# Kernel optimization log

Measured on AMD Instinct MI355X. Metric: run time of the kernel, lower is better.

Reference implementation:

```python
import jax, jax.numpy as jnp
import numpy as np

Q = 10        # icosahedral diamonds
M = 128       # 2**dggrid_level
L = Q * M * M # 163840 icosahedral points
KS = 9        # kernel_size / knn neighbors


def setup_inputs() -> dict:
    key = jax.random.key(0)
    k1, k2, k3, k4 = jax.random.split(key, 4)
    b, c, h, w = 1, 128, 256, 512
    x = jax.random.normal(k1, (b, c, h, w), dtype=jnp.float32)
    codeskmin = jax.random.randint(k2, (L, KS), 0, h * w, dtype=jnp.int32)
    att_w = jax.random.normal(k3, (KS, 2, KS), dtype=jnp.float32) * 0.1
    att_b = jnp.zeros((KS,), dtype=jnp.float32)
    depth_w = jax.random.normal(k4, (c, KS), dtype=jnp.float32) * 0.1
    depth_b = jnp.zeros((c,), dtype=jnp.float32)
    gamma = jnp.ones((c,), dtype=jnp.float32)
    beta = jnp.zeros((c,), dtype=jnp.float32)
    return {"x": x, "codeskmin": codeskmin, "att_w": att_w, "att_b": att_b,
            "depth_w": depth_w, "depth_b": depth_b, "gamma": gamma, "beta": beta}


def reference(x, codeskmin, att_w, att_b, depth_w, depth_b, gamma, beta):
    b, c, h, w = x.shape
    xf = x.reshape(b, c, h * w)
    # KNN gather: (b, c, L, KS)
    xe = xf[:, :, codeskmin]
    # --- SpatialAttentionModule_v1 ---
    avg = jnp.mean(xe, axis=1)           # (b, L, KS)
    mx = jnp.max(xe, axis=1)             # (b, L, KS)
    feat = jnp.stack([avg, mx], axis=1)  # (b, 2, L, KS)
    # Conv2d(2 -> KS, kernel (1,KS), no pad): reduces neighbor axis fully
    att = jnp.einsum('bilk,oik->bol', feat, att_w) + att_b[None, :, None]  # (b, KS, L)
    att = jax.nn.sigmoid(att)
    att = att.transpose(0, 2, 1)[:, None, :, :]  # (b, 1, L, KS)
    xe = att * xe + xe
    # --- depthwise conv over neighbor axis ---
    out = jnp.einsum('bclk,ck->bcl', xe, depth_w) + depth_b[None, :, None]  # (b, c, L)
    # rearrange 'b c (q h w) -> (b q) c h w'
    out = out.reshape(b, c, Q, M, M).transpose(0, 2, 1, 3, 4).reshape(b * Q, c, M, M)
    # BatchNorm (training-mode batch stats)
    mean = jnp.mean(out, axis=(0, 2, 3), keepdims=True)
    var = jnp.var(out, axis=(0, 2, 3), keepdims=True)
    out = (out - mean) * jax.lax.rsqrt(var + 1e-5)
    out = out * gamma[None, :, None, None] + beta[None, :, None, None]
    # Swish
    out = out * jax.nn.sigmoid(out)
    return out
```

## Files before the change

### kernel.cpp

```cpp
#include <hip/hip_runtime.h>
#include <hip/hip_bf16.h>

#define HW 131072
#define NCH 128
#define KS 9
#define L_TOTAL 163840
#define NGRP 8
#define LPB 256

typedef float        f32x2 __attribute__((ext_vector_type(2)));
typedef float        f32x4 __attribute__((ext_vector_type(4)));
typedef unsigned int u32x2 __attribute__((ext_vector_type(2)));
typedef unsigned int u32x4 __attribute__((ext_vector_type(4)));

static __device__ __forceinline__ float bflo(unsigned int p) { return __uint_as_float(p << 16); }
static __device__ __forceinline__ float bfhi(unsigned int p) { return __uint_as_float(p & 0xffff0000u); }
static __device__ __forceinline__ unsigned short f2bf(float f) {
    unsigned int x = __float_as_uint(f);
    return (unsigned short)((x + 0x7fffu + ((x >> 16) & 1u)) >> 16);
}

__global__ __launch_bounds__(256) void transpose_x_kernel(
    const f32x4* __restrict__ xf4,
    unsigned int* __restrict__ xT,
    float2* __restrict__ meanmaxP)
{
    __shared__ unsigned short tile[128 * 128];
    __shared__ float ps[8][128];
    __shared__ float pm[8][128];
    const int tid = threadIdx.x;
    const int p0 = blockIdx.x * 128;
    const int pj = tid & 31;
    const int cg = tid >> 5;

    float s0 = 0.f, s1 = 0.f, s2 = 0.f, s3 = 0.f;
    float m0 = -3.4e38f, m1 = -3.4e38f, m2 = -3.4e38f, m3 = -3.4e38f;
    #pragma unroll 4
    for (int it = 0; it < 16; ++it) {
        const int c = cg + (it << 3);
        const f32x4 v = __builtin_nontemporal_load(&xf4[(long)c * (HW / 4) + (p0 >> 2) + pj]);
        const int pA = 4 * pj;
        tile[(pA + 0) * 128 + ((c + 2 * (pA + 0)) & 127)] = f2bf(v.x);
        tile[(pA + 1) * 128 + ((c + 2 * (pA + 1)) & 127)] = f2bf(v.y);
        tile[(pA + 2) * 128 + ((c + 2 * (pA + 2)) & 127)] = f2bf(v.z);
        tile[(pA + 3) * 128 + ((c + 2 * (pA + 3)) & 127)] = f2bf(v.w);
        s0 += v.x; s1 += v.y; s2 += v.z; s3 += v.w;
        m0 = fmaxf(m0, v.x); m1 = fmaxf(m1, v.y);
        m2 = fmaxf(m2, v.z); m3 = fmaxf(m3, v.w);
    }
    {
        const int pA = 4 * pj;
        ps[cg][pA + 0] = s0; ps[cg][pA + 1] = s1;
        ps[cg][pA + 2] = s2; ps[cg][pA + 3] = s3;
        pm[cg][pA + 0] = m0; pm[cg][pA + 1] = m1;
        pm[cg][pA + 2] = m2; pm[cg][pA + 3] = m3;
    }
    __syncthreads();

    #pragma unroll 4
    for (int it = 0; it < 16; ++it) {
        const int idx2 = it * 256 + tid;
        const int s = idx2 >> 9;
        const int rem = idx2 & 511;
        const int p = rem >> 2;
        const int dp = rem & 3;
        const int cpair = s * 8 + 2 * dp;
        const int col0 = (2 * cpair + 2 * p) & 127;
        const int col1 = (2 * cpair + 2 + 2 * p) & 127;
        u32x2 u;
        u.x = *reinterpret_cast<const unsigned int*>(&tile[p * 128 + col0]);
        u.y = *reinterpret_cast<const unsigned int*>(&tile[p * 128 + col1]);
        *(u32x2*)&xT[((long)s * HW + (p0 + p)) * 8 + 2 * dp] = u;
    }
    if (tid < 128) {
        float s = 0.f, m = -3.4e38f;
        #pragma unroll
        for (int g2 = 0; g2 < 8; ++g2) {
            s += ps[g2][tid];
            m = fmaxf(m, pm[g2][tid]);
        }
        meanmaxP[p0 + tid] = make_float2(s * 0.0078125f, m);
    }
}

__global__ __launch_bounds__(256) void mult_kernel(
    const float2* __restrict__ meanmaxP,
    const int* __restrict__ cks,
    const float* __restrict__ att_w,
    const float* __restrict__ att_b,
    unsigned int* __restrict__ rec,
    float* __restrict__ gz)
{
    __shared__ float attw[162];
    __shared__ float attb[12];
    __shared__ __align__(16) unsigned int lrec[256 * 12];
    const int tid = threadIdx.x;
    const int base_l = blockIdx.x * 256;

    if (blockIdx.x == 0) gz[tid] = 0.f;

    if (tid < 162) attw[tid] = att_w[tid];
    if (tid < KS) attb[tid] = att_b[tid];
    for (int j = tid; j < 256 * KS; j += 256) {
        const int lj = j / KS;
        lrec[lj * 12 + (j - lj * KS)] = (unsigned int)cks[(long)base_l * KS + j];
    }
    __syncthreads();

    unsigned int idx[KS];
    float mean[KS], mx[KS];
    #pragma unroll
    for (int k = 0; k < KS; ++k) {
        idx[k] = lrec[tid * 12 + k];
        const float2 mm = meanmaxP[idx[k]];
        mean[k] = mm.x; mx[k] = mm.y;
    }
    #pragma unroll
    for (int o = 0; o < KS; ++o) {
        float logit = attb[o];
        #pragma unroll
        for (int k = 0; k < KS; ++k) {
            logit = fmaf(mean[k], attw[o * 18 + k], logit);
            logit = fmaf(mx[k],   attw[o * 18 + 9 + k], logit);
        }
        const float sig = 1.0f / (1.0f + __expf(-logit));
        unsigned int u = (unsigned int)(sig * 32768.0f + 0.5f);
        if (u > 32767u) u = 32767u;
        lrec[tid * 12 + o] = idx[o] | (u << 17);
    }
    __syncthreads();

    const u32x4* lv = (const u32x4*)lrec;
    u32x4* dst = (u32x4*)(rec + (size_t)base_l * 12);
    #pragma unroll
    for (int j = 0; j < 3; ++j)
        dst[j * 256 + tid] = lv[j * 256 + tid];
}

__global__ __launch_bounds__(256, 4) void gather_kernel(
    const unsigned int* __restrict__ xT,
    const unsigned int* __restrict__ rec,
    const float* __restrict__ depth_w,
    const float* __restrict__ depth_b,
    unsigned int* __restrict__ ybuf,
    float* __restrict__ gsum, float* __restrict__ gsq)
{
    __shared__ float dwl[KS][16];
    __shared__ float dbl[16];
    __shared__ float redx[4][4][8];
    __shared__ __align__(16) unsigned short ytile[16][264];

    const int tid  = threadIdx.x;
    const int lane = tid & 63;
    const int wave = tid >> 6;
    const int g      = blockIdx.x & 7;
    const int base_l = (blockIdx.x >> 3) * LPB;
    const int qt = lane & 3;
    const int lq = lane >> 2;

    if (tid < 144) {
        int k = tid >> 4, ch = tid & 15;
        dwl[k][ch] = depth_w[(g * 16 + ch) * KS + k];
    }
    if (tid < 16) dbl[tid] = depth_b[g * 16 + tid];
    __syncthreads();

    f32x2 dw[KS][2];
    #pragma unroll
    for (int k = 0; k < KS; ++k) {
        f32x4 t = *(const f32x4*)&dwl[k][qt * 4];
        dw[k][0].x = t.x; dw[k][0].y = t.y;
        dw[k][1].x = t.z; dw[k][1].y = t.w;
    }
    f32x2 db01, db23;
    {
        f32x4 t = *(const f32x4*)&dbl[qt * 4];
        db01.x = t.x; db01.y = t.y; db23.x = t.z; db23.y = t.w;
    }

    const unsigned int* slab = xT + ((size_t)g << 20);

    f32x2 sum01 = {0.f, 0.f}, sum23 = {0.f, 0.f};
    f32x2 sq01  = {0.f, 0.f}, sq23  = {0.f, 0.f};

    #pragma unroll
    for (int b = 0; b < 4; ++b) {
        const int lloc = wave * 64 + b * 16 + lq;
        const unsigned int* rp = rec + (size_t)(base_l + lloc) * 12;
        const u32x4 r0 = __builtin_nontemporal_load((const u32x4*)rp);
        const u32x4 r1 = __builtin_nontemporal_load((const u32x4*)(rp + 4));
        const unsigned int r8 = __builtin_nontemporal_load(rp + 8);
        const unsigned int rr[KS] = {r0.x, r0.y, r0.z, r0.w,
                                     r1.x, r1.y, r1.z, r1.w, r8};

        u32x2 pv[KS];
        #pragma unroll
        for (int k = 0; k < KS; ++k)
            pv[k] = *(const u32x2*)(slab + ((rr[k] & 0x1FFFFu) << 3) + (qt << 1));

        f32x2 acc01 = db01, acc23 = db23;
        #pragma unroll
        for (int k = 0; k < KS; ++k) {
            const float mk = fmaf((float)(rr[k] >> 17), 3.0517578125e-5f, 1.0f);
            f32x2 mk2; mk2.x = mk; mk2.y = mk;
            f32x2 xa; xa.x = bflo(pv[k].x); xa.y = bfhi(pv[k].x);
            f32x2 xb; xb.x = bflo(pv[k].y); xb.y = bfhi(pv[k].y);
            acc01 = __builtin_elementwise_fma(xa * mk2, dw[k][0], acc01);
            acc23 = __builtin_elementwise_fma(xb * mk2, dw[k][1], acc23);
        }

        ytile[qt * 4 + 0][lloc] = f2bf(acc01.x);
        ytile[qt * 4 + 1][lloc] = f2bf(acc01.y);
        ytile[qt * 4 + 2][lloc] = f2bf(acc23.x);
        ytile[qt * 4 + 3][lloc] = f2bf(acc23.y);

        sum01 += acc01; sum23 += acc23;
        sq01 = __builtin_elementwise_fma(acc01, acc01, sq01);
        sq23 = __builtin_elementwise_fma(acc23, acc23, sq23);
    }

    __syncthreads();

    {
        const int ch = tid >> 4;
        const int m  = tid & 15;
        const u32x4 v0 = *(const u32x4*)&ytile[ch][m * 16];
        const u32x4 v1 = *(const u32x4*)&ytile[ch][m * 16 + 8];
        unsigned int* dst = ybuf + (size_t)(g * 16 + ch) * (L_TOTAL / 2)
                          + (base_l >> 1) + m * 8;
        *(u32x4*)dst = v0;
        *(u32x4*)(dst + 4) = v1;
    }

    #pragma unroll
    for (int s = 4; s <= 32; s <<= 1) {
        sum01.x += __shfl_xor(sum01.x, s);
        sum01.y += __shfl_xor(sum01.y, s);
        sum23.x += __shfl_xor(sum23.x, s);
        sum23.y += __shfl_xor(sum23.y, s);
        sq01.x  += __shfl_xor(sq01.x,  s);
        sq01.y  += __shfl_xor(sq01.y,  s);
        sq23.x  += __shfl_xor(sq23.x,  s);
        sq23.y  += __shfl_xor(sq23.y,  s);
    }
    if (lane < 4) {
        float* rw = &redx[wave][lane][0];
        rw[0] = sum01.x; rw[1] = sum01.y; rw[2] = sum23.x; rw[3] = sum23.y;
        rw[4] = sq01.x;  rw[5] = sq01.y;  rw[6] = sq23.x;  rw[7] = sq23.y;
    }
    __syncthreads();
    if (tid < 32) {
        const int q = tid >> 2, qq = tid & 3;
        float s = redx[0][qq][q] + redx[1][qq][q] + redx[2][qq][q] + redx[3][qq][q];
        const int ch = g * 16 + qq * 4 + (q & 3);
        float* dst = (q >= 4) ? gsq : gsum;
        atomicAdd(&dst[ch], s);
    }
}

__global__ __launch_bounds__(256) void finalize_kernel(
    const u32x4* __restrict__ ybuf,
    const float* __restrict__ gsum, const float* __restrict__ gsq,
    const float* __restrict__ gamma, const float* __restrict__ beta,
    float* __restrict__ out)
{
    const int q = blockIdx.x >> 7;
    const int c = blockIdx.x & 127;
    const int tid = threadIdx.x;

    const float invN = 1.0f / (float)L_TOTAL;
    const float m = gsum[c] * invN;
    const float var = gsq[c] * invN - m * m;
    const float sc = gamma[c] * rsqrtf(var + 1e-5f);
    const float sh = beta[c] - m * sc;

    const u32x4* src = ybuf + (size_t)c * (L_TOTAL / 8) + (size_t)q * 2048;
    float* dst = out + ((size_t)(q * NCH + c) << 14);

    #pragma unroll 2
    for (int it = 0; it < 8; ++it) {
        const int i = it * 256 + tid;
        const u32x4 v = src[i];
        f32x4 o0, o1;
        float z;
        z = fmaf(bflo(v.x), sc, sh); o0.x = z / (1.0f + __expf(-z));
        z = fmaf(bfhi(v.x), sc, sh); o0.y = z / (1.0f + __expf(-z));
        z = fmaf(bflo(v.y), sc, sh); o0.z = z / (1.0f + __expf(-z));
        z = fmaf(bfhi(v.y), sc, sh); o0.w = z / (1.0f + __expf(-z));
        z = fmaf(bflo(v.z), sc, sh); o1.x = z / (1.0f + __expf(-z));
        z = fmaf(bfhi(v.z), sc, sh); o1.y = z / (1.0f + __expf(-z));
        z = fmaf(bflo(v.w), sc, sh); o1.z = z / (1.0f + __expf(-z));
        z = fmaf(bfhi(v.w), sc, sh); o1.w = z / (1.0f + __expf(-z));
        *(f32x4*)&dst[i * 8 + 0] = o0;
        *(f32x4*)&dst[i * 8 + 4] = o1;
    }
}

extern "C" void kernel_launch(void* const* d_in, const int* in_sizes, int n_in,
                              void* d_out, int out_size, void* d_ws, size_t ws_size,
                              hipStream_t stream) {
    const f32x4* x_f4  = (const f32x4*)d_in[0];
    const int* cks     = (const int*)d_in[1];
    const float* aw    = (const float*)d_in[2];
    const float* ab    = (const float*)d_in[3];
    const float* dw    = (const float*)d_in[4];
    const float* db    = (const float*)d_in[5];
    const float* gm    = (const float*)d_in[6];
    const float* bt    = (const float*)d_in[7];

    char* ws = (char*)d_ws;
    unsigned int* xT   = (unsigned int*)ws;
    float2* meanmaxP   = (float2*)(ws + 33554432);
    unsigned int* ybuf = (unsigned int*)(ws + 34603008);
    unsigned int* rec  = (unsigned int*)(ws + 76546048);
    float* gsum        = (float*)(ws + 84410368);
    float* gsq         = gsum + NCH;

    transpose_x_kernel<<<HW / 128, 256, 0, stream>>>(x_f4, xT, meanmaxP);
    mult_kernel<<<L_TOTAL / 256, 256, 0, stream>>>(meanmaxP, cks, aw, ab, rec, gsum);
    gather_kernel<<<(L_TOTAL / LPB) * NGRP, 256, 0, stream>>>(
        xT, rec, dw, db, ybuf, gsum, gsq);
    finalize_kernel<<<1280, 256, 0, stream>>>(
        (const u32x4*)ybuf, gsum, gsq, gm, bt, (float*)d_out);
}
```

Baseline: 280.6 us.

## Merge four kernels into two cooperative persistent kernels with grid sync

```diff
diff --git a/kernel.cpp b/kernel.cpp
--- a/kernel.cpp
+++ b/kernel.cpp
@@ -1,5 +1,8 @@
 #include <hip/hip_runtime.h>
 #include <hip/hip_bf16.h>
+#include <hip/hip_cooperative_groups.h>
+
+namespace cooperative_groups_ns = cooperative_groups;
 
 #define HW 131072
 #define NCH 128
@@ -20,130 +23,150 @@
     return (unsigned short)((x + 0x7fffu + ((x >> 16) & 1u)) >> 16);
 }
 
-__global__ __launch_bounds__(256) void transpose_x_kernel(
+__global__ __launch_bounds__(256, 2) void prep_kernel(
     const f32x4* __restrict__ xf4,
     unsigned int* __restrict__ xT,
-    float2* __restrict__ meanmaxP)
-{
-    __shared__ unsigned short tile[128 * 128];
-    __shared__ float ps[8][128];
-    __shared__ float pm[8][128];
-    const int tid = threadIdx.x;
-    const int p0 = blockIdx.x * 128;
-    const int pj = tid & 31;
-    const int cg = tid >> 5;
-
-    float s0 = 0.f, s1 = 0.f, s2 = 0.f, s3 = 0.f;
-    float m0 = -3.4e38f, m1 = -3.4e38f, m2 = -3.4e38f, m3 = -3.4e38f;
-    #pragma unroll 4
-    for (int it = 0; it < 16; ++it) {
-        const int c = cg + (it << 3);
-        const f32x4 v = __builtin_nontemporal_load(&xf4[(long)c * (HW / 4) + (p0 >> 2) + pj]);
-        const int pA = 4 * pj;
-        tile[(pA + 0) * 128 + ((c + 2 * (pA + 0)) & 127)] = f2bf(v.x);
-        tile[(pA + 1) * 128 + ((c + 2 * (pA + 1)) & 127)] = f2bf(v.y);
-        tile[(pA + 2) * 128 + ((c + 2 * (pA + 2)) & 127)] = f2bf(v.z);
-        tile[(pA + 3) * 128 + ((c + 2 * (pA + 3)) & 127)] = f2bf(v.w);
-        s0 += v.x; s1 += v.y; s2 += v.z; s3 += v.w;
-        m0 = fmaxf(m0, v.x); m1 = fmaxf(m1, v.y);
-        m2 = fmaxf(m2, v.z); m3 = fmaxf(m3, v.w);
-    }
-    {
-        const int pA = 4 * pj;
-        ps[cg][pA + 0] = s0; ps[cg][pA + 1] = s1;
-        ps[cg][pA + 2] = s2; ps[cg][pA + 3] = s3;
-        pm[cg][pA + 0] = m0; pm[cg][pA + 1] = m1;
-        pm[cg][pA + 2] = m2; pm[cg][pA + 3] = m3;
-    }
-    __syncthreads();
-
-    #pragma unroll 4
-    for (int it = 0; it < 16; ++it) {
-        const int idx2 = it * 256 + tid;
-        const int s = idx2 >> 9;
-        const int rem = idx2 & 511;
-        const int p = rem >> 2;
-        const int dp = rem & 3;
-        const int cpair = s * 8 + 2 * dp;
-        const int col0 = (2 * cpair + 2 * p) & 127;
-        const int col1 = (2 * cpair + 2 + 2 * p) & 127;
-        u32x2 u;
-        u.x = *reinterpret_cast<const unsigned int*>(&tile[p * 128 + col0]);
-        u.y = *reinterpret_cast<const unsigned int*>(&tile[p * 128 + col1]);
-        *(u32x2*)&xT[((long)s * HW + (p0 + p)) * 8 + 2 * dp] = u;
-    }
-    if (tid < 128) {
-        float s = 0.f, m = -3.4e38f;
-        #pragma unroll
-        for (int g2 = 0; g2 < 8; ++g2) {
-            s += ps[g2][tid];
-            m = fmaxf(m, pm[g2][tid]);
-        }
-        meanmaxP[p0 + tid] = make_float2(s * 0.0078125f, m);
-    }
-}
-
-__global__ __launch_bounds__(256) void mult_kernel(
-    const float2* __restrict__ meanmaxP,
+    float2* __restrict__ meanmaxP,
     const int* __restrict__ cks,
     const float* __restrict__ att_w,
     const float* __restrict__ att_b,
     unsigned int* __restrict__ rec,
-    float* __restrict__ gz)
+    float* __restrict__ gz,
+    int mode)
 {
-    __shared__ float attw[162];
-    __shared__ float attb[12];
-    __shared__ __align__(16) unsigned int lrec[256 * 12];
+    __shared__ __align__(16) char smem[36864];
     const int tid = threadIdx.x;
-    const int base_l = blockIdx.x * 256;
-
-    if (blockIdx.x == 0) gz[tid] = 0.f;
-
-    if (tid < 162) attw[tid] = att_w[tid];
-    if (tid < KS) attb[tid] = att_b[tid];
-    for (int j = tid; j < 256 * KS; j += 256) {
-        const int lj = j / KS;
-        lrec[lj * 12 + (j - lj * KS)] = (unsigned int)cks[(long)base_l * KS + j];
-    }
-    __syncthreads();
-
-    unsigned int idx[KS];
-    float mean[KS], mx[KS];
-    #pragma unroll
-    for (int k = 0; k < KS; ++k) {
-        idx[k] = lrec[tid * 12 + k];
-        const float2 mm = meanmaxP[idx[k]];
-        mean[k] = mm.x; mx[k] = mm.y;
-    }
-    #pragma unroll
-    for (int o = 0; o < KS; ++o) {
-        float logit = attb[o];
-        #pragma unroll
-        for (int k = 0; k < KS; ++k) {
-            logit = fmaf(mean[k], attw[o * 18 + k], logit);
-            logit = fmaf(mx[k],   attw[o * 18 + 9 + k], logit);
-        }
-        const float sig = 1.0f / (1.0f + __expf(-logit));
-        unsigned int u = (unsigned int)(sig * 32768.0f + 0.5f);
-        if (u > 32767u) u = 32767u;
-        lrec[tid * 12 + o] = idx[o] | (u << 17);
-    }
-    __syncthreads();
-
-    const u32x4* lv = (const u32x4*)lrec;
-    u32x4* dst = (u32x4*)(rec + (size_t)base_l * 12);
-    #pragma unroll
-    for (int j = 0; j < 3; ++j)
-        dst[j * 256 + tid] = lv[j * 256 + tid];
+
+    if (mode != 1) {
+        unsigned short* tile = (unsigned short*)smem;
+        float* ps = (float*)(smem + 32768);
+        float* pm = (float*)(smem + 34816);
+        const int pj = tid & 31;
+        const int cgi = tid >> 5;
+        const int wave = tid >> 6;
+
+        if (blockIdx.x == 0) gz[tid] = 0.f;
+
+        for (int tt = 0; tt < 2; ++tt) {
+            const int p0 = (blockIdx.x * 2 + tt) * 128;
+
+            float s0 = 0.f, s1 = 0.f, s2 = 0.f, s3 = 0.f;
+            float m0 = -3.4e38f, m1 = -3.4e38f, m2 = -3.4e38f, m3 = -3.4e38f;
+            #pragma unroll 4
+            for (int it = 0; it < 16; ++it) {
+                const int c = cgi + (it << 3);
+                const f32x4 v = __builtin_nontemporal_load(
+                    &xf4[(long)c * (HW / 4) + (p0 >> 2) + pj]);
+                const int pA = 4 * pj;
+                tile[(pA + 0) * 128 + ((c + 2 * (pA + 0)) & 127)] = f2bf(v.x);
+                tile[(pA + 1) * 128 + ((c + 2 * (pA + 1)) & 127)] = f2bf(v.y);
+                tile[(pA + 2) * 128 + ((c + 2 * (pA + 2)) & 127)] = f2bf(v.z);
+                tile[(pA + 3) * 128 + ((c + 2 * (pA + 3)) & 127)] = f2bf(v.w);
+                s0 += v.x; s1 += v.y; s2 += v.z; s3 += v.w;
+                m0 = fmaxf(m0, v.x); m1 = fmaxf(m1, v.y);
+                m2 = fmaxf(m2, v.z); m3 = fmaxf(m3, v.w);
+            }
+            s0 += __shfl_xor(s0, 32); s1 += __shfl_xor(s1, 32);
+            s2 += __shfl_xor(s2, 32); s3 += __shfl_xor(s3, 32);
+            m0 = fmaxf(m0, __shfl_xor(m0, 32)); m1 = fmaxf(m1, __shfl_xor(m1, 32));
+            m2 = fmaxf(m2, __shfl_xor(m2, 32)); m3 = fmaxf(m3, __shfl_xor(m3, 32));
+            if ((tid & 32) == 0) {
+                const int pA = 4 * pj;
+                ps[wave * 128 + pA + 0] = s0; ps[wave * 128 + pA + 1] = s1;
+                ps[wave * 128 + pA + 2] = s2; ps[wave * 128 + pA + 3] = s3;
+                pm[wave * 128 + pA + 0] = m0; pm[wave * 128 + pA + 1] = m1;
+                pm[wave * 128 + pA + 2] = m2; pm[wave * 128 + pA + 3] = m3;
+            }
+            __syncthreads();
+
+            #pragma unroll 4
+            for (int it = 0; it < 16; ++it) {
+                const int idx2 = it * 256 + tid;
+                const int s = idx2 >> 9;
+                const int rem = idx2 & 511;
+                const int p = rem >> 2;
+                const int dp = rem & 3;
+                const int cpair = s * 8 + 2 * dp;
+                const int col0 = (2 * cpair + 2 * p) & 127;
+                const int col1 = (2 * cpair + 2 + 2 * p) & 127;
+                u32x2 u;
+                u.x = *reinterpret_cast<const unsigned int*>(&tile[p * 128 + col0]);
+                u.y = *reinterpret_cast<const unsigned int*>(&tile[p * 128 + col1]);
+                *(u32x2*)&xT[((long)s * HW + (p0 + p)) * 8 + 2 * dp] = u;
+            }
+            if (tid < 128) {
+                float s = ps[0 * 128 + tid] + ps[1 * 128 + tid]
+                        + ps[2 * 128 + tid] + ps[3 * 128 + tid];
+                float m = fmaxf(fmaxf(pm[0 * 128 + tid], pm[1 * 128 + tid]),
+                                fmaxf(pm[2 * 128 + tid], pm[3 * 128 + tid]));
+                meanmaxP[p0 + tid] = make_float2(s * 0.0078125f, m);
+            }
+            __syncthreads();
+        }
+    }
+
+    if (mode == 2)
+        cooperative_groups_ns::this_grid().sync();
+
+    if (mode != 0) {
+        float* attw = (float*)smem;
+        float* attb = (float*)(smem + 648);
+        unsigned int* lrec = (unsigned int*)(smem + 704);
+        const int base_l = blockIdx.x * 320;
+
+        if (tid < 162) attw[tid] = att_w[tid];
+        if (tid < KS) attb[tid] = att_b[tid];
+        for (int j = tid; j < 320 * KS; j += 256) {
+            const int lj = j / KS;
+            lrec[lj * 12 + (j - lj * KS)] = (unsigned int)cks[(long)base_l * KS + j];
+        }
+        __syncthreads();
+
+        for (int lb = 0; lb < 320; lb += 256) {
+            const int ll = lb + tid;
+            if (ll < 320) {
+                unsigned int idx[KS];
+                float mean[KS], mx[KS];
+                #pragma unroll
+                for (int k = 0; k < KS; ++k) {
+                    idx[k] = lrec[ll * 12 + k];
+                    const float2 mm = meanmaxP[idx[k]];
+                    mean[k] = mm.x; mx[k] = mm.y;
+                }
+                #pragma unroll
+                for (int o = 0; o < KS; ++o) {
+                    float logit = attb[o];
+                    #pragma unroll
+                    for (int k = 0; k < KS; ++k) {
+                        logit = fmaf(mean[k], attw[o * 18 + k], logit);
+                        logit = fmaf(mx[k],   attw[o * 18 + 9 + k], logit);
+                    }
+                    const float sig = 1.0f / (1.0f + __expf(-logit));
+                    unsigned int u = (unsigned int)(sig * 32768.0f + 0.5f);
+                    if (u > 32767u) u = 32767u;
+                    lrec[ll * 12 + o] = idx[o] | (u << 17);
+                }
+            }
+        }
+        __syncthreads();
+
+        const u32x4* lv = (const u32x4*)lrec;
+        u32x4* dst = (u32x4*)(rec + (size_t)base_l * 12);
+        for (int j = tid; j < 960; j += 256)
+            dst[j] = lv[j];
+    }
 }
 
-__global__ __launch_bounds__(256, 4) void gather_kernel(
+__global__ __launch_bounds__(256, 4) void gatherfin_kernel(
     const unsigned int* __restrict__ xT,
     const unsigned int* __restrict__ rec,
     const float* __restrict__ depth_w,
     const float* __restrict__ depth_b,
     unsigned int* __restrict__ ybuf,
-    float* __restrict__ gsum, float* __restrict__ gsq)
+    float* __restrict__ gsum, float* __restrict__ gsq,
+    const float* __restrict__ gamma, const float* __restrict__ beta,
+    float* __restrict__ out,
+    int mode)
 {
     __shared__ float dwl[KS][16];
     __shared__ float dbl[16];
@@ -153,146 +176,156 @@
     const int tid  = threadIdx.x;
     const int lane = tid & 63;
     const int wave = tid >> 6;
-    const int g      = blockIdx.x & 7;
-    const int base_l = (blockIdx.x >> 3) * LPB;
+    const int g = blockIdx.x & 7;
     const int qt = lane & 3;
     const int lq = lane >> 2;
 
-    if (tid < 144) {
-        int k = tid >> 4, ch = tid & 15;
-        dwl[k][ch] = depth_w[(g * 16 + ch) * KS + k];
-    }
-    if (tid < 16) dbl[tid] = depth_b[g * 16 + tid];
-    __syncthreads();
-
-    f32x2 dw[KS][2];
-    #pragma unroll
-    for (int k = 0; k < KS; ++k) {
-        f32x4 t = *(const f32x4*)&dwl[k][qt * 4];
-        dw[k][0].x = t.x; dw[k][0].y = t.y;
-        dw[k][1].x = t.z; dw[k][1].y = t.w;
-    }
-    f32x2 db01, db23;
-    {
-        f32x4 t = *(const f32x4*)&dbl[qt * 4];
-        db01.x = t.x; db01.y = t.y; db23.x = t.z; db23.y = t.w;
-    }
-
-    const unsigned int* slab = xT + ((size_t)g << 20);
-
-    f32x2 sum01 = {0.f, 0.f}, sum23 = {0.f, 0.f};
-    f32x2 sq01  = {0.f, 0.f}, sq23  = {0.f, 0.f};
-
-    #pragma unroll
-    for (int b = 0; b < 4; ++b) {
-        const int lloc = wave * 64 + b * 16 + lq;
-        const unsigned int* rp = rec + (size_t)(base_l + lloc) * 12;
-        const u32x4 r0 = __builtin_nontemporal_load((const u32x4*)rp);
-        const u32x4 r1 = __builtin_nontemporal_load((const u32x4*)(rp + 4));
-        const unsigned int r8 = __builtin_nontemporal_load(rp + 8);
-        const unsigned int rr[KS] = {r0.x, r0.y, r0.z, r0.w,
-                                     r1.x, r1.y, r1.z, r1.w, r8};
-
-        u32x2 pv[KS];
-        #pragma unroll
-        for (int k = 0; k < KS; ++k)
-            pv[k] = *(const u32x2*)(slab + ((rr[k] & 0x1FFFFu) << 3) + (qt << 1));
-
-        f32x2 acc01 = db01, acc23 = db23;
+    if (mode != 1) {
+        if (tid < 144) {
+            int k = tid >> 4, ch = tid & 15;
+            dwl[k][ch] = depth_w[(g * 16 + ch) * KS + k];
+        }
+        if (tid < 16) dbl[tid] = depth_b[g * 16 + tid];
+        __syncthreads();
+
+        f32x2 dw[KS][2];
         #pragma unroll
         for (int k = 0; k < KS; ++k) {
-            const float mk = fmaf((float)(rr[k] >> 17), 3.0517578125e-5f, 1.0f);
-            f32x2 mk2; mk2.x = mk; mk2.y = mk;
-            f32x2 xa; xa.x = bflo(pv[k].x); xa.y = bfhi(pv[k].x);
-            f32x2 xb; xb.x = bflo(pv[k].y); xb.y = bfhi(pv[k].y);
-            acc01 = __builtin_elementwise_fma(xa * mk2, dw[k][0], acc01);
-            acc23 = __builtin_elementwise_fma(xb * mk2, dw[k][1], acc23);
-        }
-
-        ytile[qt * 4 + 0][lloc] = f2bf(acc01.x);
-        ytile[qt * 4 + 1][lloc] = f2bf(acc01.y);
-        ytile[qt * 4 + 2][lloc] = f2bf(acc23.x);
-        ytile[qt * 4 + 3][lloc] = f2bf(acc23.y);
-
-        sum01 += acc01; sum23 += acc23;
-        sq01 = __builtin_elementwise_fma(acc01, acc01, sq01);
-        sq23 = __builtin_elementwise_fma(acc23, acc23, sq23);
-    }
-
-    __syncthreads();
-
-    {
-        const int ch = tid >> 4;
-        const int m  = tid & 15;
-        const u32x4 v0 = *(const u32x4*)&ytile[ch][m * 16];
-        const u32x4 v1 = *(const u32x4*)&ytile[ch][m * 16 + 8];
-        unsigned int* dst = ybuf + (size_t)(g * 16 + ch) * (L_TOTAL / 2)
-                          + (base_l >> 1) + m * 8;
-        *(u32x4*)dst = v0;
-        *(u32x4*)(dst + 4) = v1;
-    }
-
-    #pragma unroll
-    for (int s = 4; s <= 32; s <<= 1) {
-        sum01.x += __shfl_xor(sum01.x, s);
-        sum01.y += __shfl_xor(sum01.y, s);
-        sum23.x += __shfl_xor(sum23.x, s);
-        sum23.y += __shfl_xor(sum23.y, s);
-        sq01.x  += __shfl_xor(sq01.x,  s);
-        sq01.y  += __shfl_xor(sq01.y,  s);
-        sq23.x  += __shfl_xor(sq23.x,  s);
-        sq23.y  += __shfl_xor(sq23.y,  s);
-    }
-    if (lane < 4) {
-        float* rw = &redx[wave][lane][0];
-        rw[0] = sum01.x; rw[1] = sum01.y; rw[2] = sum23.x; rw[3] = sum23.y;
-        rw[4] = sq01.x;  rw[5] = sq01.y;  rw[6] = sq23.x;  rw[7] = sq23.y;
-    }
-    __syncthreads();
-    if (tid < 32) {
-        const int q = tid >> 2, qq = tid & 3;
-        float s = redx[0][qq][q] + redx[1][qq][q] + redx[2][qq][q] + redx[3][qq][q];
-        const int ch = g * 16 + qq * 4 + (q & 3);
-        float* dst = (q >= 4) ? gsq : gsum;
-        atomicAdd(&dst[ch], s);
-    }
-}
-
-__global__ __launch_bounds__(256) void finalize_kernel(
-    const u32x4* __restrict__ ybuf,
-    const float* __restrict__ gsum, const float* __restrict__ gsq,
-    const float* __restrict__ gamma, const float* __restrict__ beta,
-    float* __restrict__ out)
-{
-    const int q = blockIdx.x >> 7;
-    const int c = blockIdx.x & 127;
-    const int tid = threadIdx.x;
-
-    const float invN = 1.0f / (float)L_TOTAL;
-    const float m = gsum[c] * invN;
-    const float var = gsq[c] * invN - m * m;
-    const float sc = gamma[c] * rsqrtf(var + 1e-5f);
-    const float sh = beta[c] - m * sc;
-
-    const u32x4* src = ybuf + (size_t)c * (L_TOTAL / 8) + (size_t)q * 2048;
-    float* dst = out + ((size_t)(q * NCH + c) << 14);
-
-    #pragma unroll 2
-    for (int it = 0; it < 8; ++it) {
-        const int i = it * 256 + tid;
-        const u32x4 v = src[i];
-        f32x4 o0, o1;
-        float z;
-        z = fmaf(bflo(v.x), sc, sh); o0.x = z / (1.0f + __expf(-z));
-        z = fmaf(bfhi(v.x), sc, sh); o0.y = z / (1.0f + __expf(-z));
-        z = fmaf(bflo(v.y), sc, sh); o0.z = z / (1.0f + __expf(-z));
-        z = fmaf(bfhi(v.y), sc, sh); o0.w = z / (1.0f + __expf(-z));
-        z = fmaf(bflo(v.z), sc, sh); o1.x = z / (1.0f + __expf(-z));
-        z = fmaf(bfhi(v.z), sc, sh); o1.y = z / (1.0f + __expf(-z));
-        z = fmaf(bflo(v.w), sc, sh); o1.z = z / (1.0f + __expf(-z));
-        z = fmaf(bfhi(v.w), sc, sh); o1.w = z / (1.0f + __expf(-z));
-        *(f32x4*)&dst[i * 8 + 0] = o0;
-        *(f32x4*)&dst[i * 8 + 4] = o1;
+            f32x4 t = *(const f32x4*)&dwl[k][qt * 4];
+            dw[k][0].x = t.x; dw[k][0].y = t.y;
+            dw[k][1].x = t.z; dw[k][1].y = t.w;
+        }
+        f32x2 db01, db23;
+        {
+            f32x4 t = *(const f32x4*)&dbl[qt * 4];
+            db01.x = t.x; db01.y = t.y; db23.x = t.z; db23.y = t.w;
+        }
+
+        const unsigned int* slab = xT + ((size_t)g << 20);
+
+        f32x2 sum01 = {0.f, 0.f}, sum23 = {0.f, 0.f};
+        f32x2 sq01  = {0.f, 0.f}, sq23  = {0.f, 0.f};
+
+        for (int t = 0; t < 5; ++t) {
+            const int base_l = ((blockIdx.x >> 3) + t * 128) * LPB;
+
+            #pragma unroll
+            for (int bq = 0; bq < 4; ++bq) {
+                const int lloc = wave * 64 + bq * 16 + lq;
+                const unsigned int* rp = rec + (size_t)(base_l + lloc) * 12;
+                const u32x4 r0 = __builtin_nontemporal_load((const u32x4*)rp);
+                const u32x4 r1 = __builtin_nontemporal_load((const u32x4*)(rp + 4));
+                const unsigned int r8 = __builtin_nontemporal_load(rp + 8);
+                const unsigned int rr[KS] = {r0.x, r0.y, r0.z, r0.w,
+                                             r1.x, r1.y, r1.z, r1.w, r8};
+
+                u32x2 pv[KS];
+                #pragma unroll
+                for (int k = 0; k < KS; ++k)
+                    pv[k] = *(const u32x2*)(slab + ((rr[k] & 0x1FFFFu) << 3) + (qt << 1));
+
+                f32x2 acc01 = db01, acc23 = db23;
+                #pragma unroll
+                for (int k = 0; k < KS; ++k) {
+                    const float mk = fmaf((float)(rr[k] >> 17), 3.0517578125e-5f, 1.0f);
+                    f32x2 mk2; mk2.x = mk; mk2.y = mk;
+                    f32x2 xa; xa.x = bflo(pv[k].x); xa.y = bfhi(pv[k].x);
+                    f32x2 xb; xb.x = bflo(pv[k].y); xb.y = bfhi(pv[k].y);
+                    acc01 = __builtin_elementwise_fma(xa * mk2, dw[k][0], acc01);
+                    acc23 = __builtin_elementwise_fma(xb * mk2, dw[k][1], acc23);
+                }
+
+                ytile[qt * 4 + 0][lloc] = f2bf(acc01.x);
+                ytile[qt * 4 + 1][lloc] = f2bf(acc01.y);
+                ytile[qt * 4 + 2][lloc] = f2bf(acc23.x);
+                ytile[qt * 4 + 3][lloc] = f2bf(acc23.y);
+
+                sum01 += acc01; sum23 += acc23;
+                sq01 = __builtin_elementwise_fma(acc01, acc01, sq01);
+                sq23 = __builtin_elementwise_fma(acc23, acc23, sq23);
+            }
+
+            __syncthreads();
+
+            {
+                const int ch = tid >> 4;
+                const int m  = tid & 15;
+                const u32x4 v0 = *(const u32x4*)&ytile[ch][m * 16];
+                const u32x4 v1 = *(const u32x4*)&ytile[ch][m * 16 + 8];
+                unsigned int* dst = ybuf + (size_t)(g * 16 + ch) * (L_TOTAL / 2)
+                                  + (base_l >> 1) + m * 8;
+                *(u32x4*)dst = v0;
+                *(u32x4*)(dst + 4) = v1;
+            }
+            __syncthreads();
+        }
+
+        #pragma unroll
+        for (int s = 4; s <= 32; s <<= 1) {
+            sum01.x += __shfl_xor(sum01.x, s);
+            sum01.y += __shfl_xor(sum01.y, s);
+            sum23.x += __shfl_xor(sum23.x, s);
+            sum23.y += __shfl_xor(sum23.y, s);
+            sq01.x  += __shfl_xor(sq01.x,  s);
+            sq01.y  += __shfl_xor(sq01.y,  s);
+            sq23.x  += __shfl_xor(sq23.x,  s);
+            sq23.y  += __shfl_xor(sq23.y,  s);
+        }
+        if (lane < 4) {
+            float* rw = &redx[wave][lane][0];
+            rw[0] = sum01.x; rw[1] = sum01.y; rw[2] = sum23.x; rw[3] = sum23.y;
+            rw[4] = sq01.x;  rw[5] = sq01.y;  rw[6] = sq23.x;  rw[7] = sq23.y;
+        }
+        __syncthreads();
+        if (tid < 32) {
+            const int q = tid >> 2, qq = tid & 3;
+            float s = redx[0][qq][q] + redx[1][qq][q] + redx[2][qq][q] + redx[3][qq][q];
+            const int ch = g * 16 + qq * 4 + (q & 3);
+            float* dst = (q >= 4) ? gsq : gsum;
+            atomicAdd(&dst[ch], s);
+        }
+    }
+
+    if (mode == 2)
+        cooperative_groups_ns::this_grid().sync();
+
+    if (mode != 0) {
+        const float invN = 1.0f / (float)L_TOTAL;
+        const int r = blockIdx.x >> 3;
+        #pragma unroll
+        for (int pass = 0; pass < 2; ++pass) {
+            const int rr2 = r + pass * 128;
+            if (rr2 < 160) {
+                const int q = rr2 >> 4;
+                const int c = g * 16 + (rr2 & 15);
+                const float m = gsum[c] * invN;
+                const float var = gsq[c] * invN - m * m;
+                const float sc = gamma[c] * rsqrtf(var + 1e-5f);
+                const float sh = beta[c] - m * sc;
+
+                const u32x4* src = (const u32x4*)ybuf + (size_t)c * (L_TOTAL / 8)
+                                 + (size_t)q * 2048;
+                float* dst = out + ((size_t)(q * NCH + c) << 14);
+
+                #pragma unroll 2
+                for (int it = 0; it < 8; ++it) {
+                    const int i = it * 256 + tid;
+                    const u32x4 v = src[i];
+                    f32x4 o0, o1;
+                    float z;
+                    z = fmaf(bflo(v.x), sc, sh); o0.x = z / (1.0f + __expf(-z));
+                    z = fmaf(bfhi(v.x), sc, sh); o0.y = z / (1.0f + __expf(-z));
+                    z = fmaf(bflo(v.y), sc, sh); o0.z = z / (1.0f + __expf(-z));
+                    z = fmaf(bfhi(v.y), sc, sh); o0.w = z / (1.0f + __expf(-z));
+                    z = fmaf(bflo(v.z), sc, sh); o1.x = z / (1.0f + __expf(-z));
+                    z = fmaf(bfhi(v.z), sc, sh); o1.y = z / (1.0f + __expf(-z));
+                    z = fmaf(bflo(v.w), sc, sh); o1.z = z / (1.0f + __expf(-z));
+                    z = fmaf(bfhi(v.w), sc, sh); o1.w = z / (1.0f + __expf(-z));
+                    *(f32x4*)&dst[i * 8 + 0] = o0;
+                    *(f32x4*)&dst[i * 8 + 4] = o1;
+                }
+            }
+        }
     }
 }
 
@@ -315,11 +348,34 @@
     unsigned int* rec  = (unsigned int*)(ws + 76546048);
     float* gsum        = (float*)(ws + 84410368);
     float* gsq         = gsum + NCH;
-
-    transpose_x_kernel<<<HW / 128, 256, 0, stream>>>(x_f4, xT, meanmaxP);
-    mult_kernel<<<L_TOTAL / 256, 256, 0, stream>>>(meanmaxP, cks, aw, ab, rec, gsum);
-    gather_kernel<<<(L_TOTAL / LPB) * NGRP, 256, 0, stream>>>(
-        xT, rec, dw, db, ybuf, gsum, gsq);
-    finalize_kernel<<<1280, 256, 0, stream>>>(
-        (const u32x4*)ybuf, gsum, gsq, gm, bt, (float*)d_out);
+    float* outp        = (float*)d_out;
+
+    int mode2 = 2;
+    void* argsP[] = {(void*)&x_f4, (void*)&xT, (void*)&meanmaxP, (void*)&cks,
+                     (void*)&aw, (void*)&ab, (void*)&rec, (void*)&gsum,
+                     (void*)&mode2};
+    hipError_t e = hipLaunchCooperativeKernel((void*)prep_kernel,
+                                              dim3(512), dim3(256),
+                                              argsP, 0, stream);
+    if (e == hipSuccess) {
+        void* argsG[] = {(void*)&xT, (void*)&rec, (void*)&dw, (void*)&db,
+                         (void*)&ybuf, (void*)&gsum, (void*)&gsq,
+                         (void*)&gm, (void*)&bt, (void*)&outp, (void*)&mode2};
+        e = hipLaunchCooperativeKernel((void*)gatherfin_kernel,
+                                       dim3(1024), dim3(256),
+                                       argsG, 0, stream);
+        if (e == hipSuccess) return;
+        gatherfin_kernel<<<1024, 256, 0, stream>>>(
+            xT, rec, dw, db, ybuf, gsum, gsq, gm, bt, outp, 0);
+        gatherfin_kernel<<<1024, 256, 0, stream>>>(
+            xT, rec, dw, db, ybuf, gsum, gsq, gm, bt, outp, 1);
+        return;
+    }
+
+    prep_kernel<<<512, 256, 0, stream>>>(x_f4, xT, meanmaxP, cks, aw, ab, rec, gsum, 0);
+    prep_kernel<<<512, 256, 0, stream>>>(x_f4, xT, meanmaxP, cks, aw, ab, rec, gsum, 1);
+    gatherfin_kernel<<<1024, 256, 0, stream>>>(
+        xT, rec, dw, db, ybuf, gsum, gsq, gm, bt, outp, 0);
+    gatherfin_kernel<<<1024, 256, 0, stream>>>(
+        xT, rec, dw, db, ybuf, gsum, gsq, gm, bt, outp, 1);
 }
```

New measurement: 517.1 us. +84.3%, slower.
